# Performance work log

Hardware: AMD Instinct MI355X
Metric: run time of the kernel (lower is better)

## Reference

```python
import jax, jax.numpy as jnp
import numpy as np

B, K, E, L, H, ENS = 32768, 5, 16, 128, 3, 3

def setup_inputs() -> dict:
    key = jax.random.key(0)
    ks = jax.random.split(key, 16)
    w = lambda i, shape: (jax.random.normal(ks[i], shape, jnp.float32) * 0.05)
    return {
        "z": jax.random.normal(ks[0], (B, L), jnp.float32),
        "anchors": jax.random.normal(ks[1], (B, K, 2), jnp.float32),
        # anchor_embed MLP: Linear(2,E) -> ReLU -> Linear(E,E)
        "W1": w(2, (E, 2)), "b1": w(3, (E,)),
        "W2": w(4, (E, E)), "b2": w(5, (E,)),
        # LSTMCell(E, L): gates order i,f,g,o
        "W_ih": w(6, (4 * L, E)), "W_hh": w(7, (4 * L, L)),
        "b_ih": w(8, (4 * L,)), "b_hh": w(9, (4 * L,)),
        # progress head Linear(L,1)
        "Wp": w(10, (1, L)), "bp": w(11, (1,)),
        # risk ensemble: ENS stacked Linear(L,1)
        "Wr": w(12, (ENS, L)), "br": w(13, (ENS,)),
    }

def reference(z, anchors, W1, b1, W2, b2, W_ih, W_hh, b_ih, b_hh, Wp, bp, Wr, br):
    Bc, Kc, _ = anchors.shape
    # anchor embedding MLP (B,K,2) -> (B,K,E)
    emb = jnp.maximum(anchors @ W1.T + b1, 0.0) @ W2.T + b2
    inp = emb.reshape(Bc * Kc, -1)                      # (B*K, E)
    h = jnp.broadcast_to(z[:, None, :], (Bc, Kc, z.shape[-1])).reshape(Bc * Kc, -1)
    c = jnp.zeros_like(h)
    x_proj = inp @ W_ih.T + b_ih                        # input projection constant over steps
    for _ in range(H):  # fixed small rollout horizon
        gates = x_proj + h @ W_hh.T + b_hh              # (B*K, 4L)
        i_g, f_g, g_g, o_g = jnp.split(gates, 4, axis=-1)
        i_g = jax.nn.sigmoid(i_g)
        f_g = jax.nn.sigmoid(f_g)
        g_g = jnp.tanh(g_g)
        o_g = jax.nn.sigmoid(o_g)
        c = f_g * c + i_g * g_g
        h = o_g * jnp.tanh(c)
    h = h.reshape(Bc, Kc, -1)                           # (B,K,L)
    progress = (h @ Wp.T + bp)[..., 0]                  # (B,K)
    risks = jnp.einsum('bkl,el->ebk', h, Wr) + br[:, None, None]  # (ENS,B,K)
    risk_mean = risks.mean(axis=0)
    unc = jnp.var(jax.nn.sigmoid(risks), axis=0, ddof=1)  # torch .var is unbiased
    return risk_mean, progress, unc, risks
```

## Files before the change

### kernel.cpp

```cpp
#include <hip/hip_runtime.h>

#define BN 32768
#define KN 5
#define LN 128
#define HN 3
#define ROWS (BN*KN)
#define BK ROWS
#define MT 64
#define TILES (ROWS/MT)
#define WGS 512
#define TPW (TILES/WGS)
#define THREADS 512
#define ASTR 168

using bf16x8 = __attribute__((ext_vector_type(8))) __bf16;
using f32x4  = __attribute__((ext_vector_type(4))) float;
using u16x8  = __attribute__((ext_vector_type(8))) unsigned short;

__device__ inline unsigned short f2bf(float x) {
    union { float f; unsigned u; } v; v.f = x;
    unsigned r = v.u + 0x7FFFu + ((v.u >> 16) & 1u);
    return (unsigned short)(r >> 16);
}
__device__ inline float bf2f(unsigned short b) {
    union { unsigned u; float f; } v; v.u = ((unsigned)b) << 16; return v.f;
}
__device__ inline float sigm(float x) {
    return __builtin_amdgcn_rcpf(1.0f + __builtin_amdgcn_exp2f(-1.44269504089f * x));
}
__device__ inline float tanh_(float x) {
    return 1.0f - 2.0f * __builtin_amdgcn_rcpf(1.0f + __builtin_amdgcn_exp2f(2.88539008178f * x));
}
__device__ inline f32x4 splat4(float x) { f32x4 r; r[0]=x; r[1]=x; r[2]=x; r[3]=x; return r; }

__global__ __launch_bounds__(THREADS, 2)
void wahead_kernel(const float* __restrict__ z,   const float* __restrict__ anchors,
                   const float* __restrict__ W1,  const float* __restrict__ b1,
                   const float* __restrict__ W2,  const float* __restrict__ b2,
                   const float* __restrict__ Wih, const float* __restrict__ Whh,
                   const float* __restrict__ bih, const float* __restrict__ bhh,
                   const float* __restrict__ Wp,  const float* __restrict__ bp,
                   const float* __restrict__ Wr,  const float* __restrict__ br,
                   float* __restrict__ out)
{
    __shared__ unsigned short sA[2 * MT * ASTR];
    __shared__ float sW1[32], sb1[16], sW2[16 * 17], sb2[16], sWp[128], sWr[384];

    const int tid  = threadIdx.x;
    const int wv   = tid >> 6;
    const int lane = tid & 63;
    const int quad = lane >> 4;
    const int cc   = lane & 15;

    if (tid < 32)  sW1[tid] = W1[tid];
    if (tid < 16)  { sb1[tid] = b1[tid]; sb2[tid] = b2[tid]; }
    if (tid < 256) sW2[(tid >> 4) * 17 + (tid & 15)] = W2[tid];
    if (tid < 128) sWp[tid] = Wp[tid];
    if (tid < 384) sWr[tid] = Wr[tid];

    bf16x8 Bf[4][5];
    float  biasv[4];
    #pragma unroll
    for (int t = 0; t < 4; ++t) {
        const int n = t * 128 + wv * 16 + cc;
        biasv[t] = bih[n] + bhh[n];
        #pragma unroll
        for (int kt = 0; kt < 5; ++kt) {
            const int k0 = kt * 32 + quad * 8;
            float v[8];
            if (k0 < 16) {
                const float4 p0 = *reinterpret_cast<const float4*>(Wih + n * 16 + k0);
                const float4 p1 = *reinterpret_cast<const float4*>(Wih + n * 16 + k0 + 4);
                v[0]=p0.x; v[1]=p0.y; v[2]=p0.z; v[3]=p0.w;
                v[4]=p1.x; v[5]=p1.y; v[6]=p1.z; v[7]=p1.w;
            } else if (k0 < 144) {
                const float4 p0 = *reinterpret_cast<const float4*>(Whh + n * 128 + (k0 - 16));
                const float4 p1 = *reinterpret_cast<const float4*>(Whh + n * 128 + (k0 - 16) + 4);
                v[0]=p0.x; v[1]=p0.y; v[2]=p0.z; v[3]=p0.w;
                v[4]=p1.x; v[5]=p1.y; v[6]=p1.z; v[7]=p1.w;
            } else {
                #pragma unroll
                for (int j = 0; j < 8; ++j) v[j] = 0.0f;
            }
            union { bf16x8 bv; unsigned short us[8]; } pk;
            #pragma unroll
            for (int j = 0; j < 8; ++j) pk.us[j] = f2bf(v[j]);
            Bf[t][kt] = pk.bv;
        }
    }

    const float bpv = bp[0];
    const float br0 = br[0], br1 = br[1], br2 = br[2];

    __syncthreads();

    const int erow = tid >> 3;
    const int esub = tid & 7;

    for (int ti = 0; ti < TPW; ++ti) {
        const int tile = blockIdx.x * TPW + ti;
        const int r0g  = tile * MT;

        {
            const int gr = r0g + erow;
            const float ax = anchors[gr * 2], ay = anchors[gr * 2 + 1];
            const int e0 = esub * 2;
            float a0 = sb2[e0], a1 = sb2[e0 + 1];
            #pragma unroll
            for (int hh = 0; hh < 16; ++hh) {
                float pre = fmaf(sW1[hh * 2], ax, fmaf(sW1[hh * 2 + 1], ay, sb1[hh]));
                pre = fmaxf(pre, 0.0f);
                a0 = fmaf(pre, sW2[e0 * 17 + hh], a0);
                a1 = fmaf(pre, sW2[(e0 + 1) * 17 + hh], a1);
            }
            const unsigned short b0 = f2bf(a0), b1v = f2bf(a1);
            #pragma unroll
            for (int bufi = 0; bufi < 2; ++bufi) {
                unsigned short* row = &sA[bufi * MT * ASTR + erow * ASTR];
                row[e0]     = b0;  row[e0 + 1]     = b1v;
                row[144 + e0] = 0; row[144 + e0 + 1] = 0;
            }
            const unsigned b_idx = (unsigned)gr / 5u;
            const float4* zp = reinterpret_cast<const float4*>(z + (size_t)b_idx * 128 + esub * 16);
            const float4 z0 = zp[0], z1 = zp[1], z2 = zp[2], z3 = zp[3];
            union { u16x8 v; unsigned short us[8]; } w0, w1;
            w0.us[0]=f2bf(z0.x); w0.us[1]=f2bf(z0.y); w0.us[2]=f2bf(z0.z); w0.us[3]=f2bf(z0.w);
            w0.us[4]=f2bf(z1.x); w0.us[5]=f2bf(z1.y); w0.us[6]=f2bf(z1.z); w0.us[7]=f2bf(z1.w);
            w1.us[0]=f2bf(z2.x); w1.us[1]=f2bf(z2.y); w1.us[2]=f2bf(z2.z); w1.us[3]=f2bf(z2.w);
            w1.us[4]=f2bf(z3.x); w1.us[5]=f2bf(z3.y); w1.us[6]=f2bf(z3.z); w1.us[7]=f2bf(z3.w);
            unsigned short* hrow = &sA[erow * ASTR + 16 + esub * 16];
            *reinterpret_cast<u16x8*>(hrow)     = w0.v;
            *reinterpret_cast<u16x8*>(hrow + 8) = w1.v;
        }

        float cst[4][4] = {{0,0,0,0},{0,0,0,0},{0,0,0,0},{0,0,0,0}};

        #pragma unroll
        for (int s = 0; s < HN; ++s) {
            const int cur = s & 1;
            const int nxt = cur ^ 1;
            __syncthreads();

            #pragma unroll
            for (int mt = 0; mt < 4; ++mt) {
                f32x4 acc[4];
                #pragma unroll
                for (int t = 0; t < 4; ++t) acc[t] = splat4(biasv[t]);

                #pragma unroll
                for (int kt = 0; kt < 5; ++kt) {
                    const bf16x8 a = *reinterpret_cast<const bf16x8*>(
                        &sA[cur * MT * ASTR + (mt * 16 + cc) * ASTR + kt * 32 + quad * 8]);
                    #pragma unroll
                    for (int t = 0; t < 4; ++t)
                        acc[t] = __builtin_amdgcn_mfma_f32_16x16x32_bf16(a, Bf[t][kt], acc[t], 0, 0, 0);
                }
                const int lcol = wv * 16 + cc;
                #pragma unroll
                for (int r = 0; r < 4; ++r) {
                    const float ig = sigm(acc[0][r]);
                    const float fg = sigm(acc[1][r]);
                    const float gg = tanh_(acc[2][r]);
                    const float og = sigm(acc[3][r]);
                    const float cn = fmaf(fg, cst[mt][r], ig * gg);
                    cst[mt][r] = cn;
                    const float hn = og * tanh_(cn);
                    const int m = mt * 16 + quad * 4 + r;
                    sA[nxt * MT * ASTR + m * ASTR + 16 + lcol] = f2bf(hn);
                }
            }
        }

        __syncthreads();

        {
            const int row = tid >> 3;
            const int j   = tid & 7;
            const unsigned short* hrow = &sA[1 * MT * ASTR + row * ASTR + 16 + j * 16];
            const u16x8 h0 = *reinterpret_cast<const u16x8*>(hrow);
            const u16x8 h1 = *reinterpret_cast<const u16x8*>(hrow + 8);
            float p = 0.f, q0 = 0.f, q1 = 0.f, q2 = 0.f;
            #pragma unroll
            for (int u = 0; u < 16; ++u) {
                const int l = j * 16 + u;
                const float hv = bf2f(u < 8 ? h0[u] : h1[u - 8]);
                p  = fmaf(hv, sWp[l], p);
                q0 = fmaf(hv, sWr[l], q0);
                q1 = fmaf(hv, sWr[128 + l], q1);
                q2 = fmaf(hv, sWr[256 + l], q2);
            }
            #pragma unroll
            for (int m = 1; m < 8; m <<= 1) {
                p  += __shfl_xor(p,  m, 64);
                q0 += __shfl_xor(q0, m, 64);
                q1 += __shfl_xor(q1, m, 64);
                q2 += __shfl_xor(q2, m, 64);
            }
            if (j == 0) {
                const int gr = r0g + row;
                const float prog  = p + bpv;
                const float rr0 = q0 + br0, rr1 = q1 + br1, rr2 = q2 + br2;
                const float rmean = (rr0 + rr1 + rr2) * (1.0f / 3.0f);
                const float s0 = sigm(rr0), s1 = sigm(rr1), s2 = sigm(rr2);
                const float sm = (s0 + s1 + s2) * (1.0f / 3.0f);
                const float d0 = s0 - sm, d1 = s1 - sm, d2 = s2 - sm;
                const float unc = (d0 * d0 + d1 * d1 + d2 * d2) * 0.5f;
                out[gr]          = rmean;
                out[BK + gr]     = prog;
                out[2 * BK + gr] = unc;
                out[3 * BK + gr] = rr0;
                out[4 * BK + gr] = rr1;
                out[5 * BK + gr] = rr2;
            }
        }
    }
}

extern "C" void kernel_launch(void* const* d_in, const int* in_sizes, int n_in,
                              void* d_out, int out_size, void* d_ws, size_t ws_size,
                              hipStream_t stream) {
    const float* z       = (const float*)d_in[0];
    const float* anchors = (const float*)d_in[1];
    const float* W1      = (const float*)d_in[2];
    const float* b1      = (const float*)d_in[3];
    const float* W2      = (const float*)d_in[4];
    const float* b2      = (const float*)d_in[5];
    const float* Wih     = (const float*)d_in[6];
    const float* Whh     = (const float*)d_in[7];
    const float* bih     = (const float*)d_in[8];
    const float* bhh     = (const float*)d_in[9];
    const float* Wp      = (const float*)d_in[10];
    const float* bp      = (const float*)d_in[11];
    const float* Wr      = (const float*)d_in[12];
    const float* br      = (const float*)d_in[13];

    hipLaunchKernelGGL(wahead_kernel, dim3(WGS), dim3(THREADS), 0, stream,
                       z, anchors, W1, b1, W2, b2, Wih, Whh, bih, bhh,
                       Wp, bp, Wr, br, (float*)d_out);
}
```

Measured before the change: 230.9 us.

## Fold log2e into LSTM weights, merge gate reciprocals, batch MFMAs across row tiles

The gate weights and biases are pre-scaled by -log2e, or by 2·log2e for the g gate, so the MFMA outputs feed exp2 directly without extra multiplies. The cell and hidden updates are rewritten algebraically so each element needs two reciprocals instead of five. All four row-tile MFMA groups are now issued before the gate epilogue, with A fragments double-buffered from LDS, and bf16 stores use a hardware pack-convert when available. The costs are more live accumulator registers and possible overflow in the combined products for very large gate inputs.

Result: faster. 213.0 us (-7.7%).

```diff
diff --git a/kernel.cpp b/kernel.cpp
--- a/kernel.cpp
+++ b/kernel.cpp
@@ -12,8 +12,10 @@
 #define TPW (TILES/WGS)
 #define THREADS 512
 #define ASTR 168
+#define LOG2E 1.44269504089f
 
 using bf16x8 = __attribute__((ext_vector_type(8))) __bf16;
+using bf16x2 = __attribute__((ext_vector_type(2))) __bf16;
 using f32x4  = __attribute__((ext_vector_type(4))) float;
 using u16x8  = __attribute__((ext_vector_type(8))) unsigned short;
 
@@ -22,14 +24,20 @@
     unsigned r = v.u + 0x7FFFu + ((v.u >> 16) & 1u);
     return (unsigned short)(r >> 16);
 }
+#if __has_builtin(__builtin_amdgcn_cvt_pk_bf16_f32)
+__device__ inline unsigned short f2bf_fast(float x) {
+    union { bf16x2 v; unsigned short us[2]; } u;
+    u.v = __builtin_amdgcn_cvt_pk_bf16_f32(x, x);
+    return u.us[0];
+}
+#else
+__device__ inline unsigned short f2bf_fast(float x) { return f2bf(x); }
+#endif
 __device__ inline float bf2f(unsigned short b) {
     union { unsigned u; float f; } v; v.u = ((unsigned)b) << 16; return v.f;
 }
 __device__ inline float sigm(float x) {
-    return __builtin_amdgcn_rcpf(1.0f + __builtin_amdgcn_exp2f(-1.44269504089f * x));
-}
-__device__ inline float tanh_(float x) {
-    return 1.0f - 2.0f * __builtin_amdgcn_rcpf(1.0f + __builtin_amdgcn_exp2f(2.88539008178f * x));
+    return __builtin_amdgcn_rcpf(1.0f + __builtin_amdgcn_exp2f(-LOG2E * x));
 }
 __device__ inline f32x4 splat4(float x) { f32x4 r; r[0]=x; r[1]=x; r[2]=x; r[3]=x; return r; }
 
@@ -62,8 +70,9 @@
     float  biasv[4];
     #pragma unroll
     for (int t = 0; t < 4; ++t) {
+        const float sc = (t == 2) ? (2.0f * LOG2E) : (-LOG2E);
         const int n = t * 128 + wv * 16 + cc;
-        biasv[t] = bih[n] + bhh[n];
+        biasv[t] = sc * (bih[n] + bhh[n]);
         #pragma unroll
         for (int kt = 0; kt < 5; ++kt) {
             const int k0 = kt * 32 + quad * 8;
@@ -84,7 +93,7 @@
             }
             union { bf16x8 bv; unsigned short us[8]; } pk;
             #pragma unroll
-            for (int j = 0; j < 8; ++j) pk.us[j] = f2bf(v[j]);
+            for (int j = 0; j < 8; ++j) pk.us[j] = f2bf(sc * v[j]);
             Bf[t][kt] = pk.bv;
         }
     }
@@ -97,6 +106,7 @@
     const int erow = tid >> 3;
     const int esub = tid & 7;
 
+    #pragma unroll 1
     for (int ti = 0; ti < TPW; ++ti) {
         const int tile = blockIdx.x * TPW + ti;
         const int r0g  = tile * MT;
@@ -117,8 +127,8 @@
             #pragma unroll
             for (int bufi = 0; bufi < 2; ++bufi) {
                 unsigned short* row = &sA[bufi * MT * ASTR + erow * ASTR];
-                row[e0]     = b0;  row[e0 + 1]     = b1v;
-                row[144 + e0] = 0; row[144 + e0 + 1] = 0;
+                row[e0]       = b0;  row[e0 + 1]       = b1v;
+                row[144 + e0] = 0;   row[144 + e0 + 1] = 0;
             }
             const unsigned b_idx = (unsigned)gr / 5u;
             const float4* zp = reinterpret_cast<const float4*>(z + (size_t)b_idx * 128 + esub * 16);
@@ -133,7 +143,9 @@
             *reinterpret_cast<u16x8*>(hrow + 8) = w1.v;
         }
 
-        float cst[4][4] = {{0,0,0,0},{0,0,0,0},{0,0,0,0},{0,0,0,0}};
+        float cst[16];
+        #pragma unroll
+        for (int e = 0; e < 16; ++e) cst[e] = 0.0f;
 
         #pragma unroll
         for (int s = 0; s < HN; ++s) {
@@ -141,33 +153,54 @@
             const int nxt = cur ^ 1;
             __syncthreads();
 
+            f32x4 acc[4][4];
+            #pragma unroll
+            for (int mt = 0; mt < 4; ++mt)
+                #pragma unroll
+                for (int t = 0; t < 4; ++t)
+                    acc[mt][t] = splat4(biasv[t]);
+
+            bf16x8 af[2][5];
+            #pragma unroll
+            for (int kt = 0; kt < 5; ++kt)
+                af[0][kt] = *reinterpret_cast<const bf16x8*>(
+                    &sA[cur * MT * ASTR + cc * ASTR + kt * 32 + quad * 8]);
             #pragma unroll
             for (int mt = 0; mt < 4; ++mt) {
-                f32x4 acc[4];
+                const int pb = mt & 1;
+                if (mt < 3) {
+                    #pragma unroll
+                    for (int kt = 0; kt < 5; ++kt)
+                        af[pb ^ 1][kt] = *reinterpret_cast<const bf16x8*>(
+                            &sA[cur * MT * ASTR + ((mt + 1) * 16 + cc) * ASTR + kt * 32 + quad * 8]);
+                }
                 #pragma unroll
-                for (int t = 0; t < 4; ++t) acc[t] = splat4(biasv[t]);
-
-                #pragma unroll
-                for (int kt = 0; kt < 5; ++kt) {
-                    const bf16x8 a = *reinterpret_cast<const bf16x8*>(
-                        &sA[cur * MT * ASTR + (mt * 16 + cc) * ASTR + kt * 32 + quad * 8]);
+                for (int kt = 0; kt < 5; ++kt)
                     #pragma unroll
                     for (int t = 0; t < 4; ++t)
-                        acc[t] = __builtin_amdgcn_mfma_f32_16x16x32_bf16(a, Bf[t][kt], acc[t], 0, 0, 0);
-                }
-                const int lcol = wv * 16 + cc;
-                #pragma unroll
-                for (int r = 0; r < 4; ++r) {
-                    const float ig = sigm(acc[0][r]);
-                    const float fg = sigm(acc[1][r]);
-                    const float gg = tanh_(acc[2][r]);
-                    const float og = sigm(acc[3][r]);
-                    const float cn = fmaf(fg, cst[mt][r], ig * gg);
-                    cst[mt][r] = cn;
-                    const float hn = og * tanh_(cn);
-                    const int m = mt * 16 + quad * 4 + r;
-                    sA[nxt * MT * ASTR + m * ASTR + 16 + lcol] = f2bf(hn);
-                }
+                        acc[mt][t] = __builtin_amdgcn_mfma_f32_16x16x32_bf16(
+                            af[pb][kt], Bf[t][kt], acc[mt][t], 0, 0, 0);
+            }
+
+            const int lcol = wv * 16 + cc;
+            #pragma unroll
+            for (int e = 0; e < 16; ++e) {
+                const int mt = e >> 2, r = e & 3;
+                const float Ei = __builtin_amdgcn_exp2f(acc[mt][0][r]);
+                const float Ef = __builtin_amdgcn_exp2f(acc[mt][1][r]);
+                const float Eg = __builtin_amdgcn_exp2f(acc[mt][2][r]);
+                const float Eo = __builtin_amdgcn_exp2f(acc[mt][3][r]);
+                const float t1  = (1.0f + Ei) * (1.0f + Eg);
+                const float ef1 = 1.0f + Ef;
+                const float t3  = (Eg - 1.0f) * ef1;
+                const float num = fmaf(cst[e], t1, t3);
+                const float cn  = num * __builtin_amdgcn_rcpf(t1 * ef1);
+                cst[e] = cn;
+                const float Ec = __builtin_amdgcn_exp2f(2.0f * LOG2E * cn);
+                const float hn = (Ec - 1.0f) *
+                    __builtin_amdgcn_rcpf((1.0f + Eo) * (1.0f + Ec));
+                const int m = mt * 16 + quad * 4 + r;
+                sA[nxt * MT * ASTR + m * ASTR + 16 + lcol] = f2bf_fast(hn);
             }
         }
 
```
